# Kernel optimization log

Measured on AMD Instinct MI355X. Metric: run time of the kernel, lower is better.

The kernel has to match this reference:

```python
import jax, jax.numpy as jnp
import numpy as np

HID, NL, NH, DH, FF = 768, 12, 12, 64, 3072
VOCAB, MAXPOS = 30522, 512
T_ELE, T_ROLE = 17, 7
B, L = 16, 256
LN_EPS = 1e-12


def _layernorm(x, g, b):
    mu = x.mean(-1, keepdims=True)
    var = ((x - mu) ** 2).mean(-1, keepdims=True)
    return (x - mu) / jnp.sqrt(var + LN_EPS) * g + b


def _bert(datas, word_emb, pos_emb, type_emb, emb_ln_g, emb_ln_b,
          Wq, bq, Wk, bk, Wv, bv, Wo, bo, ln1_g, ln1_b,
          W1, b1, W2, b2, ln2_g, ln2_b):
    Bv, Lv = datas.shape
    x = word_emb[datas] + pos_emb[:Lv][None] + type_emb[0][None, None]
    x = _layernorm(x, emb_ln_g, emb_ln_b)
    for i in range(NL):  # loop over fixed layer count, not data dims
        q = (x @ Wq[i] + bq[i]).reshape(Bv, Lv, NH, DH)
        k = (x @ Wk[i] + bk[i]).reshape(Bv, Lv, NH, DH)
        v = (x @ Wv[i] + bv[i]).reshape(Bv, Lv, NH, DH)
        att = jax.nn.softmax(jnp.einsum('bqhd,bkhd->bhqk', q, k) / jnp.sqrt(jnp.float32(DH)), axis=-1)
        ctx = jnp.einsum('bhqk,bkhd->bqhd', att, v).reshape(Bv, Lv, HID)
        x = _layernorm(x + ctx @ Wo[i] + bo[i], ln1_g[i], ln1_b[i])
        h = jax.nn.gelu(x @ W1[i] + b1[i], approximate=False)
        x = _layernorm(x + h @ W2[i] + b2[i], ln2_g[i], ln2_b[i])
    return x


def _crf_llh(em, tags, mask, start, end, trans):
    # torchcrf CRF.forward with batch_first=True, reduction='sum'
    Bv, Lv, T = em.shape
    bidx = jnp.arange(Bv)
    em_t = jnp.transpose(em, (1, 0, 2))        # [L,B,T]
    tags_t = tags.T.astype(jnp.int32)          # [L,B]
    mask_t = mask.T.astype(em.dtype)           # [L,B]
    # numerator: score of gold path
    score = start[tags_t[0]] + em_t[0][bidx, tags_t[0]]
    def num_step(s, xs):
        e_t, tg, tp, m = xs
        return s + m * (trans[tp, tg] + e_t[bidx, tg]), None
    score, _ = jax.lax.scan(num_step, score, (em_t[1:], tags_t[1:], tags_t[:-1], mask_t[1:]))
    last_idx = (mask_t.sum(0) - 1).astype(jnp.int32)
    num = score + end[tags[bidx, last_idx]]
    # denominator: forward algorithm (log-sum-exp semiring)
    alpha = start[None] + em_t[0]              # [B,T]
    def den_step(a, xs):
        e_t, m = xs
        nxt = jax.nn.logsumexp(a[:, :, None] + trans[None] + e_t[:, None, :], axis=1)
        return jnp.where(m[:, None] > 0, nxt, a), None
    alpha, _ = jax.lax.scan(den_step, alpha, (em_t[1:], mask_t[1:]))
    den = jax.nn.logsumexp(alpha + end[None], axis=1)
    return jnp.sum(num - den)


def _crf_decode(em, start, end, trans):
    # torchcrf CRF.decode without mask -> full-length Viterbi
    Bv = em.shape[0]
    bidx = jnp.arange(Bv)
    em_t = jnp.transpose(em, (1, 0, 2))        # [L,B,T]
    alpha = start[None] + em_t[0]
    def fwd(a, e_t):
        sc = a[:, :, None] + trans[None]       # [B,T_prev,T_cur]
        return jnp.max(sc, axis=1) + e_t, jnp.argmax(sc, axis=1)
    alpha, hist = jax.lax.scan(fwd, alpha, em_t[1:])   # hist [L-1,B,T]
    last = jnp.argmax(alpha + end[None], axis=1)
    def back(cur, h):
        prev = h[bidx, cur]
        return prev, prev
    _, ys = jax.lax.scan(back, last, hist, reverse=True)  # ys[t] = tag at pos t
    return jnp.concatenate([ys, last[None]], axis=0).T    # [B,L]


def setup_inputs() -> dict:
    key = jax.random.key(0)
    ks = iter(jax.random.split(key, 64))
    n = lambda shape: jax.random.normal(next(ks), shape, dtype=jnp.float32) * 0.02
    inp = {
        'datas': jax.random.randint(next(ks), (B, L), 0, VOCAB, dtype=jnp.int32),
        'ele_labels': jax.random.randint(next(ks), (B, L), 0, T_ELE, dtype=jnp.int32),
        'role_labels': jax.random.randint(next(ks), (B, L), 0, T_ROLE, dtype=jnp.int32),
        'seq_mask': jnp.ones((B, L), dtype=bool),
        'word_emb': n((VOCAB, HID)), 'pos_emb': n((MAXPOS, HID)), 'type_emb': n((2, HID)),
        'emb_ln_g': jnp.ones((HID,)), 'emb_ln_b': jnp.zeros((HID,)),
        'Wq': n((NL, HID, HID)), 'bq': jnp.zeros((NL, HID)),
        'Wk': n((NL, HID, HID)), 'bk': jnp.zeros((NL, HID)),
        'Wv': n((NL, HID, HID)), 'bv': jnp.zeros((NL, HID)),
        'Wo': n((NL, HID, HID)), 'bo': jnp.zeros((NL, HID)),
        'ln1_g': jnp.ones((NL, HID)), 'ln1_b': jnp.zeros((NL, HID)),
        'W1': n((NL, HID, FF)), 'b1': jnp.zeros((NL, FF)),
        'W2': n((NL, FF, HID)), 'b2': jnp.zeros((NL, HID)),
        'ln2_g': jnp.ones((NL, HID)), 'ln2_b': jnp.zeros((NL, HID)),
        'W_ele': n((HID, T_ELE)), 'b_ele': jnp.zeros((T_ELE,)),
        'W_role': n((HID, T_ROLE)), 'b_role': jnp.zeros((T_ROLE,)),
        'ele_start': n((T_ELE,)), 'ele_end': n((T_ELE,)), 'ele_trans': n((T_ELE, T_ELE)),
        'role_start': n((T_ROLE,)), 'role_end': n((T_ROLE,)), 'role_trans': n((T_ROLE, T_ROLE)),
    }
    return inp


def reference(datas, ele_labels, role_labels, seq_mask,
              word_emb, pos_emb, type_emb, emb_ln_g, emb_ln_b,
              Wq, bq, Wk, bk, Wv, bv, Wo, bo, ln1_g, ln1_b,
              W1, b1, W2, b2, ln2_g, ln2_b,
              W_ele, b_ele, W_role, b_role,
              ele_start, ele_end, ele_trans, role_start, role_end, role_trans):
    wemb = _bert(datas, word_emb, pos_emb, type_emb, emb_ln_g, emb_ln_b,
                 Wq, bq, Wk, bk, Wv, bv, Wo, bo, ln1_g, ln1_b,
                 W1, b1, W2, b2, ln2_g, ln2_b)
    ele_em = wemb @ W_ele + b_ele
    role_em = wemb @ W_role + b_role
    mask = seq_mask.astype(jnp.float32)
    ele_llh = _crf_llh(ele_em, ele_labels, mask, ele_start, ele_end, ele_trans)
    role_llh = _crf_llh(role_em, role_labels, mask, role_start, role_end, role_trans)
    loss = -ele_llh - role_llh
    ele_dec = _crf_decode(ele_em, ele_start, ele_end, ele_trans)
    role_dec = _crf_decode(role_em, role_start, role_end, role_trans)
    return loss, ele_dec, role_dec
```

## Files before the change

### kernel.cpp

```cpp
#include <hip/hip_runtime.h>
#include <stdint.h>
#include <math.h>

typedef _Float16 f16;
typedef _Float16 f16x4 __attribute__((ext_vector_type(4)));
typedef _Float16 f16x8 __attribute__((ext_vector_type(8)));
typedef float f32x4 __attribute__((ext_vector_type(4)));

#define LO_SCALE 2048.0f
#define INV_LO_SCALE (1.0f/2048.0f)
#define LOG2E 1.4426950408889634f
#define MFMA16(a, b, c) __builtin_amdgcn_mfma_f32_16x16x32_f16(a, b, c, 0, 0, 0)

__device__ __forceinline__ void split1(float x, f16 &hi, f16 &lo) {
    f16 h = (f16)x;
    hi = h;
    lo = (f16)((x - (float)h) * LO_SCALE);
}

__device__ __forceinline__ float fexp2(float x) {
#if __has_builtin(__builtin_amdgcn_exp2f)
    return __builtin_amdgcn_exp2f(x);
#else
    return exp2f(x);
#endif
}
__device__ __forceinline__ float flog2(float x) {
#if __has_builtin(__builtin_amdgcn_logf)
    return __builtin_amdgcn_logf(x);
#else
    return log2f(x);
#endif
}

#define GLOAD16(g, l) __builtin_amdgcn_global_load_lds( \
    (const __attribute__((address_space(1))) void*)(g), \
    (__attribute__((address_space(3))) void*)(l), 16, 0, 0)

__device__ __forceinline__ void swz_decode(int &mi, int &ni)
{
    const int NN = gridDim.y;
    int s = blockIdx.x + blockIdx.y * gridDim.x;
    const int c = s & 7;
    const int idx = s >> 3;
    const int mchunk = gridDim.x >> 3;
    const int md = idx / NN;
    mi = c * mchunk + md;
    ni = idx - md * NN;
}

template<int EPI>
__device__ __forceinline__ void epi_write(float val, int row, int col, int N,
                                          float* __restrict__ C,
                                          f16* __restrict__ Oh, f16* __restrict__ Ol,
                                          f16* __restrict__ X2h, f16* __restrict__ X2l,
                                          f16* __restrict__ X3h, f16* __restrict__ X3l)
{
    if constexpr (EPI == 0) {
        C[(size_t)row * N + col] = val;
    } else if constexpr (EPI == 1) {
        float ge = 0.5f * val * (1.0f + erff(val * 0.70710678118654752440f));
        f16 hi, lo;
        split1(ge, hi, lo);
        size_t o = (size_t)row * N + col;
        Oh[o] = hi;
        Ol[o] = lo;
    } else {
        int sect = col >= 1536 ? 2 : (col >= 768 ? 1 : 0);
        int cc = col - sect * 768;
        int hd = cc >> 6;
        int d = cc & 63;
        int bh = (row >> 8) * 12 + hd;
        int lt = row & 255;
        f16 hi, lo;
        split1(val, hi, lo);
        if (sect == 0) {
            size_t o = ((size_t)bh * 256 + lt) * 64 + d;
            Oh[o] = hi; Ol[o] = lo;
        } else if (sect == 1) {
            size_t o = ((size_t)bh * 256 + lt) * 64 + d;
            X2h[o] = hi; X2l[o] = lo;
        } else {
            size_t o = ((size_t)bh * 64 + d) * 256 + lt;
            X3h[o] = hi; X3l[o] = lo;
        }
    }
}

template<int EPI>
__global__ __launch_bounds__(256, 2)
void gemm128(const f16* __restrict__ Ah, const f16* __restrict__ Al,
             const f16* __restrict__ Bh, const f16* __restrict__ Bl,
             const float* __restrict__ bias, float* __restrict__ C,
             f16* __restrict__ Oh, f16* __restrict__ Ol,
             f16* __restrict__ X2h, f16* __restrict__ X2l,
             f16* __restrict__ X3h, f16* __restrict__ X3l, int K, int N)
{
    __shared__ f16 smem[2][16384];

    int mi, ni;
    swz_decode(mi, ni);
    const int m0 = mi * 128;
    const int n0 = ni * 128;

    const int tid = threadIdx.x;
    const int lane = tid & 63;
    const int w = tid >> 6;
    const int l15 = lane & 15;
    const int lg = lane >> 4;

    f32x4 accm[4][4];
    f32x4 accc[4][4];
#pragma unroll
    for (int i = 0; i < 4; ++i)
#pragma unroll
        for (int j = 0; j < 4; ++j) {
            accm[i][j] = (f32x4){0.f, 0.f, 0.f, 0.f};
            accc[i][j] = (f32x4){0.f, 0.f, 0.f, 0.f};
        }

    const f16* gA0 = Ah + (size_t)(m0 + w * 32 + l15) * K + lg * 8;
    const f16* gA1 = gA0 + 16 * (size_t)K;
    const f16* gAl0 = Al + (size_t)(m0 + w * 32 + l15) * K + lg * 8;
    const f16* gAl1 = gAl0 + 16 * (size_t)K;
    const f16* gB0 = Bh + (size_t)(n0 + w * 32 + l15) * K + lg * 8;
    const f16* gB1 = gB0 + 16 * (size_t)K;
    const f16* gBl0 = Bl + (size_t)(n0 + w * 32 + l15) * K + lg * 8;
    const f16* gBl1 = gBl0 + 16 * (size_t)K;
    const int ldsb0 = w * 1024;
    const int ldsb1 = w * 1024 + 512;

    const int nt = K >> 5;

#define STAGE(buf, k0)                                   \
    {                                                    \
        f16* sb = &smem[buf][0];                         \
        GLOAD16(gA0 + (k0), sb + ldsb0);                 \
        GLOAD16(gA1 + (k0), sb + ldsb1);                 \
        GLOAD16(gAl0 + (k0), sb + 4096 + ldsb0);         \
        GLOAD16(gAl1 + (k0), sb + 4096 + ldsb1);         \
        GLOAD16(gB0 + (k0), sb + 8192 + ldsb0);          \
        GLOAD16(gB1 + (k0), sb + 8192 + ldsb1);          \
        GLOAD16(gBl0 + (k0), sb + 12288 + ldsb0);        \
        GLOAD16(gBl1 + (k0), sb + 12288 + ldsb1);        \
    }

    STAGE(0, 0);
    __syncthreads();

    const int fro = lg * 128 + l15 * 8;
    const int wrg = (w >> 1) * 4;
    const int wcg = (w & 1) * 4;

    int cur = 0;
    for (int t = 0; t < nt; ++t) {
        if (t + 1 < nt) STAGE(cur ^ 1, (t + 1) * 32);

        const f16* sb = &smem[cur][0];
        f16x8 fbh[4], fbl[4];
#pragma unroll
        for (int ni2 = 0; ni2 < 4; ++ni2) {
            int offb = 8192 + (wcg + ni2) * 512 + fro;
            fbh[ni2] = *(const f16x8*)(sb + offb);
            fbl[ni2] = *(const f16x8*)(sb + offb + 4096);
        }
#pragma unroll
        for (int mi2 = 0; mi2 < 4; ++mi2) {
            int offa = (wrg + mi2) * 512 + fro;
            f16x8 fah = *(const f16x8*)(sb + offa);
            f16x8 fal = *(const f16x8*)(sb + offa + 4096);
            __builtin_amdgcn_s_setprio(1);
#pragma unroll
            for (int ni2 = 0; ni2 < 4; ++ni2) {
                accm[mi2][ni2] = MFMA16(fah, fbh[ni2], accm[mi2][ni2]);
                accc[mi2][ni2] = MFMA16(fah, fbl[ni2], accc[mi2][ni2]);
                accc[mi2][ni2] = MFMA16(fal, fbh[ni2], accc[mi2][ni2]);
            }
            __builtin_amdgcn_s_setprio(0);
        }

        __syncthreads();
        cur ^= 1;
    }
#undef STAGE

    const int wr = (w >> 1) * 64;
    const int wc = (w & 1) * 64;
#pragma unroll
    for (int mi2 = 0; mi2 < 4; ++mi2) {
        int row = m0 + wr + mi2 * 16 + lg * 4;
#pragma unroll
        for (int ni2 = 0; ni2 < 4; ++ni2) {
            int col = n0 + wc + ni2 * 16 + l15;
            float bv = bias[col];
#pragma unroll
            for (int j = 0; j < 4; ++j) {
                float val = accm[mi2][ni2][j] + accc[mi2][ni2][j] * INV_LO_SCALE + bv;
                epi_write<EPI>(val, row + j, col, N, C, Oh, Ol, X2h, X2l, X3h, X3l);
            }
        }
    }
}

__global__ __launch_bounds__(256, 1)
void attn_mfma_kernel(const f16* __restrict__ Qh, const f16* __restrict__ Ql,
                      const f16* __restrict__ Kh, const f16* __restrict__ Kl,
                      const f16* __restrict__ Vth, const f16* __restrict__ Vtl,
                      f16* __restrict__ ch, f16* __restrict__ cl)
{
    __shared__ f16 sKh[256 * 72];
    __shared__ f16 sKl[256 * 72];
    __shared__ f16 sVh[64 * 264];
    __shared__ f16 sVl[64 * 264];
    __shared__ f16 sPh[4][1280];
    __shared__ f16 sPl[4][1280];

    const int bh = blockIdx.x >> 1;
    const int qbase = (blockIdx.x & 1) * 128;
    const int b = bh / 12;
    const int h = bh % 12;
    const int tid = threadIdx.x;
    const int w = tid >> 6;
    const int l = tid & 63;
    const int l15 = l & 15;
    const int lg = l >> 4;

    {
        const f16* gKh = Kh + (size_t)bh * 16384;
        const f16* gKl = Kl + (size_t)bh * 16384;
#pragma unroll
        for (int i = 0; i < 8; ++i) {
            int c = tid + i * 256;
            int off = (c >> 3) * 72 + (c & 7) * 8;
            *(f16x8*)(sKh + off) = *(const f16x8*)(gKh + c * 8);
            *(f16x8*)(sKl + off) = *(const f16x8*)(gKl + c * 8);
        }
        const f16* gVh = Vth + (size_t)bh * 16384;
        const f16* gVl = Vtl + (size_t)bh * 16384;
#pragma unroll
        for (int i = 0; i < 8; ++i) {
            int c = tid + i * 256;
            int off = (c >> 5) * 264 + (c & 31) * 8;
            *(f16x8*)(sVh + off) = *(const f16x8*)(gVh + c * 8);
            *(f16x8*)(sVl + off) = *(const f16x8*)(gVl + c * 8);
        }
    }
    __syncthreads();

    f16x8 qfh[2][2], qfl[2][2];
#pragma unroll
    for (int mt = 0; mt < 2; ++mt) {
        int qr = qbase + w * 32 + mt * 16 + l15;
        size_t qo = ((size_t)bh * 256 + qr) * 64 + lg * 8;
        qfh[mt][0] = *(const f16x8*)(Qh + qo);
        qfh[mt][1] = *(const f16x8*)(Qh + qo + 32);
        qfl[mt][0] = *(const f16x8*)(Ql + qo);
        qfl[mt][1] = *(const f16x8*)(Ql + qo + 32);
    }

    f32x4 S[2][16];
#pragma unroll
    for (int nt = 0; nt < 16; ++nt) {
        int kr = nt * 16 + l15;
        int kaddr = kr * 72 + lg * 8;
        f16x8 kh0 = *(const f16x8*)(sKh + kaddr);
        f16x8 kh1 = *(const f16x8*)(sKh + kaddr + 32);
        f16x8 kl0 = *(const f16x8*)(sKl + kaddr);
        f16x8 kl1 = *(const f16x8*)(sKl + kaddr + 32);
#pragma unroll
        for (int mt = 0; mt < 2; ++mt) {
            f32x4 am = (f32x4){0.f, 0.f, 0.f, 0.f};
            f32x4 ac = (f32x4){0.f, 0.f, 0.f, 0.f};
            am = MFMA16(qfh[mt][0], kh0, am);
            am = MFMA16(qfh[mt][1], kh1, am);
            ac = MFMA16(qfh[mt][0], kl0, ac);
            ac = MFMA16(qfh[mt][1], kl1, ac);
            ac = MFMA16(qfl[mt][0], kh0, ac);
            ac = MFMA16(qfl[mt][1], kh1, ac);
            S[mt][nt] = (am + ac * INV_LO_SCALE) * 0.125f;
        }
    }

#pragma unroll
    for (int mt = 0; mt < 2; ++mt)
#pragma unroll
        for (int j = 0; j < 4; ++j) {
            float m = S[mt][0][j];
#pragma unroll
            for (int nt = 1; nt < 16; ++nt) m = fmaxf(m, S[mt][nt][j]);
            m = fmaxf(m, __shfl_xor(m, 1));
            m = fmaxf(m, __shfl_xor(m, 2));
            m = fmaxf(m, __shfl_xor(m, 4));
            m = fmaxf(m, __shfl_xor(m, 8));
            float s = 0.f;
#pragma unroll
            for (int nt = 0; nt < 16; ++nt) {
                float e = fexp2((S[mt][nt][j] - m) * LOG2E);
                S[mt][nt][j] = e;
                s += e;
            }
            s += __shfl_xor(s, 1);
            s += __shfl_xor(s, 2);
            s += __shfl_xor(s, 4);
            s += __shfl_xor(s, 8);
            float inv = 1.0f / s;
#pragma unroll
            for (int nt = 0; nt < 16; ++nt) S[mt][nt][j] *= inv;
        }

    f32x4 Ohh[2][4], Occ[2][4];
#pragma unroll
    for (int mt = 0; mt < 2; ++mt)
#pragma unroll
        for (int dt = 0; dt < 4; ++dt) {
            Ohh[mt][dt] = (f32x4){0.f, 0.f, 0.f, 0.f};
            Occ[mt][dt] = (f32x4){0.f, 0.f, 0.f, 0.f};
        }

    f16* pbh = &sPh[w][0];
    f16* pbl = &sPl[w][0];
#pragma unroll
    for (int kp = 0; kp < 8; ++kp) {
#pragma unroll
        for (int mt = 0; mt < 2; ++mt)
#pragma unroll
            for (int n2 = 0; n2 < 2; ++n2) {
                int nt = kp * 2 + n2;
#pragma unroll
                for (int j = 0; j < 4; ++j) {
                    int prow = mt * 16 + lg * 4 + j;
                    int pcol = n2 * 16 + l15;
                    f16 hi, lo;
                    split1(S[mt][nt][j], hi, lo);
                    pbh[prow * 40 + pcol] = hi;
                    pbl[prow * 40 + pcol] = lo;
                }
            }
        __builtin_amdgcn_wave_barrier();
#pragma unroll
        for (int mt = 0; mt < 2; ++mt) {
            int paddr = (mt * 16 + l15) * 40 + lg * 8;
            f16x8 ph = *(const f16x8*)(pbh + paddr);
            f16x8 pl = *(const f16x8*)(pbl + paddr);
#pragma unroll
            for (int dt = 0; dt < 4; ++dt) {
                int vaddr = (dt * 16 + l15) * 264 + kp * 32 + lg * 8;
                f16x8 vh = *(const f16x8*)(sVh + vaddr);
                f16x8 vl = *(const f16x8*)(sVl + vaddr);
                Ohh[mt][dt] = MFMA16(ph, vh, Ohh[mt][dt]);
                Occ[mt][dt] = MFMA16(ph, vl, Occ[mt][dt]);
                Occ[mt][dt] = MFMA16(pl, vh, Occ[mt][dt]);
            }
        }
        __builtin_amdgcn_wave_barrier();
    }

#pragma unroll
    for (int mt = 0; mt < 2; ++mt)
#pragma unroll
        for (int dt = 0; dt < 4; ++dt) {
            f32x4 o = Ohh[mt][dt] + Occ[mt][dt] * INV_LO_SCALE;
#pragma unroll
            for (int j = 0; j < 4; ++j) {
                int q = qbase + w * 32 + mt * 16 + lg * 4 + j;
                int d = dt * 16 + l15;
                size_t off = ((size_t)(b * 256 + q)) * 768 + h * 64 + d;
                f16 hi, lo;
                split1(o[j], hi, lo);
                ch[off] = hi;
                cl[off] = lo;
            }
        }
}

__device__ __forceinline__ void tsplit_tile(const float* __restrict__ W,
                                            f16* __restrict__ Th, f16* __restrict__ Tl,
                                            int K, int N, int kb, int nb, int tid,
                                            float (*tile)[33])
{
    const int k0 = kb * 32;
    const int n0 = nb * 32;
    const int r = tid >> 3;
    const int c4 = (tid & 7) * 4;
    float4 v = *(const float4*)&W[(size_t)(k0 + r) * N + n0 + c4];
    tile[r][c4 + 0] = v.x; tile[r][c4 + 1] = v.y;
    tile[r][c4 + 2] = v.z; tile[r][c4 + 3] = v.w;
    __syncthreads();
    f16 hs[4], ls[4];
#pragma unroll
    for (int j = 0; j < 4; ++j) split1(tile[c4 + j][r], hs[j], ls[j]);
    size_t o = (size_t)(n0 + r) * K + k0 + c4;
    Th[o + 0] = hs[0]; Th[o + 1] = hs[1]; Th[o + 2] = hs[2]; Th[o + 3] = hs[3];
    Tl[o + 0] = ls[0]; Tl[o + 1] = ls[1]; Tl[o + 2] = ls[2]; Tl[o + 3] = ls[3];
}

#define OFF_QKV_H 0
#define OFF_QKV_L 1769472
#define OFF_WO_H  3538944
#define OFF_WO_L  4128768
#define OFF_W1_H  4718592
#define OFF_W1_L  7077888
#define OFF_W2_H  9437184
#define OFF_W2_L  11796480
#define WL_STRIDE 14155776

__global__ void tsplit_all_kernel(const float* __restrict__ Wq, const float* __restrict__ Wk,
                                  const float* __restrict__ Wv, const float* __restrict__ Wo,
                                  const float* __restrict__ W1, const float* __restrict__ W2,
                                  f16* __restrict__ wout, size_t outStride)
{
    __shared__ float tile[32][33];
    const int tid = threadIdx.x;
    const int layer = blockIdx.y;
    const size_t o768 = (size_t)layer * 589824;
    const size_t o3072 = (size_t)layer * 2359296;
    f16* base = wout + (size_t)layer * outStride;
    f16* qkvh = base + OFF_QKV_H;
    f16* qkvl = base + OFF_QKV_L;
    f16* woh  = base + OFF_WO_H;
    f16* wol  = base + OFF_WO_L;
    f16* w1h  = base + OFF_W1_H;
    f16* w1l  = base + OFF_W1_L;
    f16* w2h  = base + OFF_W2_H;
    f16* w2l  = base + OFF_W2_L;
    int bid = blockIdx.x;
    if (bid < 576) {
        tsplit_tile(Wq + o768, qkvh, qkvl, 768, 768, bid % 24, bid / 24, tid, tile);
    } else if (bid < 1152) {
        bid -= 576;
        tsplit_tile(Wk + o768, qkvh + 768 * 768, qkvl + 768 * 768, 768, 768, bid % 24, bid / 24, tid, tile);
    } else if (bid < 1728) {
        bid -= 1152;
        tsplit_tile(Wv + o768, qkvh + 2 * 768 * 768, qkvl + 2 * 768 * 768, 768, 768, bid % 24, bid / 24, tid, tile);
    } else if (bid < 2304) {
        bid -= 1728;
        tsplit_tile(Wo + o768, woh, wol, 768, 768, bid % 24, bid / 24, tid, tile);
    } else if (bid < 4608) {
        bid -= 2304;
        tsplit_tile(W1 + o3072, w1h, w1l, 768, 3072, bid % 24, bid / 24, tid, tile);
    } else {
        bid -= 4608;
        tsplit_tile(W2 + o3072, w2h, w2l, 3072, 768, bid % 96, bid / 96, tid, tile);
    }
}

__global__ void pack_qkv_bias_kernel(const float* __restrict__ bq, const float* __restrict__ bk,
                                     const float* __restrict__ bv, float* __restrict__ qkvb)
{
    const int i = blockIdx.x;
    const int tid = threadIdx.x;
    for (int c = tid; c < 768; c += 256) {
        qkvb[i * 2304 + c]        = bq[i * 768 + c];
        qkvb[i * 2304 + 768 + c]  = bk[i * 768 + c];
        qkvb[i * 2304 + 1536 + c] = bv[i * 768 + c];
    }
}

__device__ __forceinline__ void ln_wave_core(float v[12], const float* __restrict__ g,
                                             const float* __restrict__ be,
                                             float* __restrict__ x,
                                             f16* __restrict__ xh, f16* __restrict__ xl,
                                             size_t base, int cb)
{
    float s = 0.f;
#pragma unroll
    for (int j = 0; j < 12; ++j) s += v[j];
#pragma unroll
    for (int off = 32; off > 0; off >>= 1) s += __shfl_xor(s, off);
    const float mu = s * (1.0f / 768.0f);
    float d2 = 0.f;
#pragma unroll
    for (int j = 0; j < 12; ++j) { float d = v[j] - mu; d2 += d * d; }
#pragma unroll
    for (int off = 32; off > 0; off >>= 1) d2 += __shfl_xor(d2, off);
    const float rstd = 1.0f / sqrtf(d2 * (1.0f / 768.0f) + 1e-12f);

    const float4* ga = (const float4*)(g + cb);
    const float4* ba = (const float4*)(be + cb);
    float o[12];
#pragma unroll
    for (int j = 0; j < 3; ++j) {
        float4 gg = ga[j];
        float4 bb = ba[j];
        o[j * 4 + 0] = (v[j * 4 + 0] - mu) * rstd * gg.x + bb.x;
        o[j * 4 + 1] = (v[j * 4 + 1] - mu) * rstd * gg.y + bb.y;
        o[j * 4 + 2] = (v[j * 4 + 2] - mu) * rstd * gg.z + bb.z;
        o[j * 4 + 3] = (v[j * 4 + 3] - mu) * rstd * gg.w + bb.w;
    }
    float4* xo = (float4*)(x + base);
#pragma unroll
    for (int j = 0; j < 3; ++j)
        xo[j] = (float4){o[j * 4 + 0], o[j * 4 + 1], o[j * 4 + 2], o[j * 4 + 3]};

    f16 ho[12], lo[12];
#pragma unroll
    for (int j = 0; j < 12; ++j) split1(o[j], ho[j], lo[j]);
#pragma unroll
    for (int j = 0; j < 3; ++j) {
        *(f16x4*)(xh + base + j * 4) = (f16x4){ho[j * 4], ho[j * 4 + 1], ho[j * 4 + 2], ho[j * 4 + 3]};
        *(f16x4*)(xl + base + j * 4) = (f16x4){lo[j * 4], lo[j * 4 + 1], lo[j * 4 + 2], lo[j * 4 + 3]};
    }
}

__global__ __launch_bounds__(256)
void res_ln_w(float* __restrict__ x, const float* __restrict__ y,
              const float* __restrict__ g, const float* __restrict__ be,
              f16* __restrict__ xh, f16* __restrict__ xl)
{
    const int tok = blockIdx.x * 4 + (threadIdx.x >> 6);
    const int cb = (threadIdx.x & 63) * 12;
    const size_t base = (size_t)tok * 768 + cb;
    const float4* xa = (const float4*)(x + base);
    const float4* ya = (const float4*)(y + base);
    float v[12];
#pragma unroll
    for (int j = 0; j < 3; ++j) {
        float4 a = xa[j];
        float4 b2 = ya[j];
        v[j * 4 + 0] = a.x + b2.x;
        v[j * 4 + 1] = a.y + b2.y;
        v[j * 4 + 2] = a.z + b2.z;
        v[j * 4 + 3] = a.w + b2.w;
    }
    ln_wave_core(v, g, be, x, xh, xl, base, cb);
}

__global__ __launch_bounds__(256)
void embed_ln_w(const int* __restrict__ datas, const float* __restrict__ wemb,
                const float* __restrict__ pemb, const float* __restrict__ temb,
                const float* __restrict__ g, const float* __restrict__ be,
                float* __restrict__ x, f16* __restrict__ xh, f16* __restrict__ xl)
{
    const int tok = blockIdx.x * 4 + (threadIdx.x >> 6);
    const int cb = (threadIdx.x & 63) * 12;
    const size_t base = (size_t)tok * 768 + cb;
    const int widx = datas[tok];
    const int l = tok & 255;
    const float4* wa = (const float4*)(wemb + (size_t)widx * 768 + cb);
    const float4* pa = (const float4*)(pemb + (size_t)l * 768 + cb);
    const float4* ta = (const float4*)(temb + cb);
    float v[12];
#pragma unroll
    for (int j = 0; j < 3; ++j) {
        float4 a = wa[j];
        float4 b2 = pa[j];
        float4 c2 = ta[j];
        v[j * 4 + 0] = a.x + b2.x + c2.x;
        v[j * 4 + 1] = a.y + b2.y + c2.y;
        v[j * 4 + 2] = a.z + b2.z + c2.z;
        v[j * 4 + 3] = a.w + b2.w + c2.w;
    }
    ln_wave_core(v, g, be, x, xh, xl, base, cb);
}

__global__ void head_kernel(const float* __restrict__ X, const float* __restrict__ Wh,
                            const float* __restrict__ bh, float* __restrict__ out, int T)
{
    __shared__ float xs[768];
    __shared__ double part[8][32];
    const int i = blockIdx.x;
    const int tid = threadIdx.x;
    for (int c = tid; c < 768; c += 256) xs[c] = X[(size_t)i * 768 + c];
    __syncthreads();
    const int p = tid >> 5;
    const int tg = tid & 31;
    if (tg < T) {
        double a = 0;
        for (int d = p * 96; d < p * 96 + 96; ++d)
            a += (double)xs[d] * (double)Wh[d * T + tg];
        part[p][tg] = a;
    }
    __syncthreads();
    if (tid < T) {
        double s = 0;
        for (int pp = 0; pp < 8; ++pp) s += part[pp][tid];
        out[(size_t)i * T + tid] = (float)(s + (double)bh[tid]);
    }
}

__global__ void crf_num_kernel(const float* __restrict__ em, const int* __restrict__ labels,
                               const float* __restrict__ start, const float* __restrict__ endv,
                               const float* __restrict__ trans, float* __restrict__ num, int T)
{
    __shared__ double red[256];
    const int b = blockIdx.x;
    const int tid = threadIdx.x;
    const int tag = labels[b * 256 + tid];
    float v;
    if (tid == 0) {
        v = start[tag] + em[(size_t)(b * 256) * T + tag];
    } else {
        int pt = labels[b * 256 + tid - 1];
        v = trans[pt * T + tag] + em[(size_t)(b * 256 + tid) * T + tag];
    }
    red[tid] = (double)v;
    __syncthreads();
    for (int st = 128; st > 0; st >>= 1) { if (tid < st) red[tid] += red[tid + st]; __syncthreads(); }
    if (tid == 0) num[b] = (float)(red[0] + (double)endv[labels[b * 256 + 255]]);
}

template<int T>
__global__ void crf_scan_kernel(const float* __restrict__ emG, const float* __restrict__ start,
                                const float* __restrict__ endv, const float* __restrict__ trans,
                                float* __restrict__ den, float* __restrict__ tagOut)
{
    __shared__ float ems[256 * T];
    __shared__ float albuf[32];
    __shared__ unsigned char hist[255 * T + 1];
    const int b = blockIdx.x;
    const bool vit = (blockIdx.y == 1);
    const int c = threadIdx.x;

    for (int idx = c; idx < 256 * T; idx += 64)
        ems[idx] = emG[(size_t)b * 256 * T + idx];
    float trc[T];
#pragma unroll
    for (int p = 0; p < T; ++p) trc[p] = (c < T) ? trans[p * T + c] : 0.f;
    const float ec = (c < T) ? endv[c] : -1e30f;
    __syncthreads();

    float alpha = (c < T) ? (start[c] + ems[c]) : -1e30f;

    if (!vit) {
        for (int t = 1; t < 256; ++t) {
            if (c < T) albuf[c] = alpha;
            __builtin_amdgcn_wave_barrier();
            float a[T];
            float m = -1e30f;
#pragma unroll
            for (int p = 0; p < T; ++p) { a[p] = albuf[p] + trc[p]; m = fmaxf(m, a[p]); }
            float s = 0.f;
#pragma unroll
            for (int p = 0; p < T; ++p) s += fexp2((a[p] - m) * LOG2E);
            float na = m + flog2(s) * 0.6931471805599453f + ems[t * T + c];
            __builtin_amdgcn_wave_barrier();
            if (c < T) alpha = na;
        }
        if (c < T) albuf[c] = alpha + ec;
        __builtin_amdgcn_wave_barrier();
        if (c == 0) {
            float m = -1e30f;
            for (int p = 0; p < T; ++p) m = fmaxf(m, albuf[p]);
            float s = 0.f;
            for (int p = 0; p < T; ++p) s += fexp2((albuf[p] - m) * LOG2E);
            den[b] = m + flog2(s) * 0.6931471805599453f;
        }
    } else {
        for (int t = 1; t < 256; ++t) {
            if (c < T) albuf[c] = alpha;
            __builtin_amdgcn_wave_barrier();
            float best = albuf[0] + trc[0];
            int arg = 0;
#pragma unroll
            for (int p = 1; p < T; ++p) {
                float v2 = albuf[p] + trc[p];
                if (v2 > best) { best = v2; arg = p; }
            }
            __builtin_amdgcn_wave_barrier();
            if (c < T) {
                alpha = best + ems[t * T + c];
                hist[(t - 1) * T + c] = (unsigned char)arg;
            }
        }
        if (c < T) albuf[c] = alpha + ec;
        __builtin_amdgcn_wave_barrier();
        if (c == 0) {
            float bv = albuf[0];
            int cur = 0;
            for (int p = 1; p < T; ++p) {
                if (albuf[p] > bv) { bv = albuf[p]; cur = p; }
            }
            tagOut[b * 256 + 255] = (float)cur;
            for (int t = 254; t >= 0; --t) {
                cur = hist[t * T + cur];
                tagOut[b * 256 + t] = (float)cur;
            }
        }
    }
}

__global__ void loss_kernel(const float* __restrict__ num, const float* __restrict__ den,
                            float* __restrict__ out)
{
    __shared__ double red[32];
    const int tid = threadIdx.x;
    red[tid] = (double)num[tid] - (double)den[tid];
    __syncthreads();
    for (int st = 16; st > 0; st >>= 1) { if (tid < st) red[tid] += red[tid + st]; __syncthreads(); }
    if (tid == 0) out[0] = (float)(-red[0]);
}

extern "C" void kernel_launch(void* const* d_in, const int* in_sizes, int n_in,
                              void* d_out, int out_size, void* d_ws, size_t ws_size,
                              hipStream_t stream)
{
    (void)in_sizes; (void)n_in; (void)out_size;
    const int* datas       = (const int*)d_in[0];
    const int* ele_labels  = (const int*)d_in[1];
    const int* role_labels = (const int*)d_in[2];
    const float* word_emb = (const float*)d_in[4];
    const float* pos_emb  = (const float*)d_in[5];
    const float* type_emb = (const float*)d_in[6];
    const float* emb_g = (const float*)d_in[7];
    const float* emb_b = (const float*)d_in[8];
    const float* Wq = (const float*)d_in[9];  const float* bq = (const float*)d_in[10];
    const float* Wk = (const float*)d_in[11]; const float* bk = (const float*)d_in[12];
    const float* Wv = (const float*)d_in[13]; const float* bv = (const float*)d_in[14];
    const float* Wo = (const float*)d_in[15]; const float* bo = (const float*)d_in[16];
    const float* ln1g = (const float*)d_in[17]; const float* ln1b = (const float*)d_in[18];
    const float* W1 = (const float*)d_in[19]; const float* b1 = (const float*)d_in[20];
    const float* W2 = (const float*)d_in[21]; const float* b2 = (const float*)d_in[22];
    const float* ln2g = (const float*)d_in[23]; const float* ln2b = (const float*)d_in[24];
    const float* W_ele = (const float*)d_in[25]; const float* b_ele = (const float*)d_in[26];
    const float* W_role = (const float*)d_in[27]; const float* b_role = (const float*)d_in[28];
    const float* ele_start = (const float*)d_in[29];
    const float* ele_end   = (const float*)d_in[30];
    const float* ele_trans = (const float*)d_in[31];
    const float* role_start = (const float*)d_in[32];
    const float* role_end   = (const float*)d_in[33];
    const float* role_trans = (const float*)d_in[34];
    float* out = (float*)d_out;

    uint8_t* ws = (uint8_t*)d_ws;
    float* x      = (float*)(ws + 0x0000000);
    f16* xh       = (f16*)  (ws + 0x0C00000);
    f16* xl       = (f16*)  (ws + 0x1200000);
    f16* Qh       = (f16*)  (ws + 0x1800000);
    f16* Ql       = (f16*)  (ws + 0x1E00000);
    f16* Kh       = (f16*)  (ws + 0x2400000);
    f16* Kl       = (f16*)  (ws + 0x2A00000);
    f16* Vth      = (f16*)  (ws + 0x3000000);
    f16* Vtl      = (f16*)  (ws + 0x3600000);
    f16* ctxh     = (f16*)  (ws + 0x3C00000);
    f16* ctxl     = (f16*)  (ws + 0x4200000);
    float* rbuf   = (float*)(ws + 0x4800000);
    f16* hh       = (f16*)  (ws + 0x1800000);
    f16* hl       = (f16*)  (ws + 0x3000000);
    float* qkvb   = (float*)(ws + 0x5400000);
    float* ele_em = (float*)(ws + 0x5420000);
    float* role_em= (float*)(ws + 0x5468000);
    float* numb   = (float*)(ws + 0x5484000);
    float* denb   = (float*)(ws + 0x5484100);
    f16* wsplit   = (f16*)  (ws + 0x5490000);

    const bool hoist = ws_size >= (0x5490000ull + 12ull * WL_STRIDE * 2ull + 0x10000ull);

    pack_qkv_bias_kernel<<<12, 256, 0, stream>>>(bq, bk, bv, qkvb);
    embed_ln_w<<<1024, 256, 0, stream>>>(datas, word_emb, pos_emb, type_emb,
                                         emb_g, emb_b, x, xh, xl);
    if (hoist)
        tsplit_all_kernel<<<dim3(6912, 12), 256, 0, stream>>>(Wq, Wk, Wv, Wo, W1, W2,
                                                              wsplit, WL_STRIDE);

    for (int i = 0; i < 12; ++i) {
        if (!hoist)
            tsplit_all_kernel<<<dim3(6912, 1), 256, 0, stream>>>(
                Wq + (size_t)i * 589824, Wk + (size_t)i * 589824,
                Wv + (size_t)i * 589824, Wo + (size_t)i * 589824,
                W1 + (size_t)i * 2359296, W2 + (size_t)i * 2359296,
                wsplit, 0);
        f16* wl = wsplit + (hoist ? (size_t)i * WL_STRIDE : 0);

        gemm128<2><<<dim3(32, 18), 256, 0, stream>>>(xh, xl, wl + OFF_QKV_H, wl + OFF_QKV_L,
                                                     qkvb + i * 2304, nullptr,
                                                     Qh, Ql, Kh, Kl, Vth, Vtl, 768, 2304);
        attn_mfma_kernel<<<384, 256, 0, stream>>>(Qh, Ql, Kh, Kl, Vth, Vtl, ctxh, ctxl);
        gemm128<0><<<dim3(32, 6), 256, 0, stream>>>(ctxh, ctxl, wl + OFF_WO_H, wl + OFF_WO_L,
                                                    bo + i * 768, rbuf, nullptr, nullptr,
                                                    nullptr, nullptr, nullptr, nullptr, 768, 768);
        res_ln_w<<<1024, 256, 0, stream>>>(x, rbuf, ln1g + i * 768, ln1b + i * 768, xh, xl);
        gemm128<1><<<dim3(32, 24), 256, 0, stream>>>(xh, xl, wl + OFF_W1_H, wl + OFF_W1_L,
                                                     b1 + i * 3072, nullptr, hh, hl,
                                                     nullptr, nullptr, nullptr, nullptr, 768, 3072);
        gemm128<0><<<dim3(32, 6), 256, 0, stream>>>(hh, hl, wl + OFF_W2_H, wl + OFF_W2_L,
                                                    b2 + i * 768, rbuf, nullptr, nullptr,
                                                    nullptr, nullptr, nullptr, nullptr, 3072, 768);
        res_ln_w<<<1024, 256, 0, stream>>>(x, rbuf, ln2g + i * 768, ln2b + i * 768, xh, xl);
    }

    head_kernel<<<4096, 256, 0, stream>>>(x, W_ele, b_ele, ele_em, 17);
    head_kernel<<<4096, 256, 0, stream>>>(x, W_role, b_role, role_em, 7);

    crf_num_kernel<<<16, 256, 0, stream>>>(ele_em, ele_labels, ele_start, ele_end, ele_trans, numb, 17);
    crf_num_kernel<<<16, 256, 0, stream>>>(role_em, role_labels, role_start, role_end, role_trans, numb + 16, 7);
    crf_scan_kernel<17><<<dim3(16, 2), 64, 0, stream>>>(ele_em, ele_start, ele_end, ele_trans, denb, out + 1);
    crf_scan_kernel<7><<<dim3(16, 2), 64, 0, stream>>>(role_em, role_start, role_end, role_trans, denb + 16, out + 1 + 4096);
    loss_kernel<<<1, 32, 0, stream>>>(numb, denb, out);
}
```

Baseline: 5.507 ms.

## Move V transpose into attention smem load; use 64x64 weight split tiles

The QKV GEMM epilogue now writes V in the same row-major [bh, l, d] layout as Q and K, so its stores are no longer strided. The attention kernel transposes V while copying it into shared memory, using scalar LDS writes. Separately, the weight transpose-and-split kernel processes 64x64 tiles per block instead of 32x32, issuing 16-byte vector stores and launching four times fewer blocks. The trade-off is scalar, possibly bank-conflicting LDS stores in attention and a larger shared tile per block in the split kernel.

```diff
diff --git a/kernel.cpp b/kernel.cpp
--- a/kernel.cpp
+++ b/kernel.cpp
@@ -74,16 +74,10 @@
         int lt = row & 255;
         f16 hi, lo;
         split1(val, hi, lo);
-        if (sect == 0) {
-            size_t o = ((size_t)bh * 256 + lt) * 64 + d;
-            Oh[o] = hi; Ol[o] = lo;
-        } else if (sect == 1) {
-            size_t o = ((size_t)bh * 256 + lt) * 64 + d;
-            X2h[o] = hi; X2l[o] = lo;
-        } else {
-            size_t o = ((size_t)bh * 64 + d) * 256 + lt;
-            X3h[o] = hi; X3l[o] = lo;
-        }
+        size_t o = ((size_t)bh * 256 + lt) * 64 + d;
+        if (sect == 0)      { Oh[o] = hi;  Ol[o] = lo; }
+        else if (sect == 1) { X2h[o] = hi; X2l[o] = lo; }
+        else                { X3h[o] = hi; X3l[o] = lo; }
     }
 }
 
@@ -205,7 +199,7 @@
 __global__ __launch_bounds__(256, 1)
 void attn_mfma_kernel(const f16* __restrict__ Qh, const f16* __restrict__ Ql,
                       const f16* __restrict__ Kh, const f16* __restrict__ Kl,
-                      const f16* __restrict__ Vth, const f16* __restrict__ Vtl,
+                      const f16* __restrict__ Vh, const f16* __restrict__ Vl,
                       f16* __restrict__ ch, f16* __restrict__ cl)
 {
     __shared__ f16 sKh[256 * 72];
@@ -235,14 +229,20 @@
             *(f16x8*)(sKh + off) = *(const f16x8*)(gKh + c * 8);
             *(f16x8*)(sKl + off) = *(const f16x8*)(gKl + c * 8);
         }
-        const f16* gVh = Vth + (size_t)bh * 16384;
-        const f16* gVl = Vtl + (size_t)bh * 16384;
+        const f16* gVh = Vh + (size_t)bh * 16384;
+        const f16* gVl = Vl + (size_t)bh * 16384;
 #pragma unroll
         for (int i = 0; i < 8; ++i) {
             int c = tid + i * 256;
-            int off = (c >> 5) * 264 + (c & 31) * 8;
-            *(f16x8*)(sVh + off) = *(const f16x8*)(gVh + c * 8);
-            *(f16x8*)(sVl + off) = *(const f16x8*)(gVl + c * 8);
+            int l2 = c >> 3;
+            int d0 = (c & 7) * 8;
+            f16x8 vh = *(const f16x8*)(gVh + l2 * 64 + d0);
+            f16x8 vl = *(const f16x8*)(gVl + l2 * 64 + d0);
+#pragma unroll
+            for (int j = 0; j < 8; ++j) {
+                sVh[(d0 + j) * 264 + l2] = vh[j];
+                sVl[(d0 + j) * 264 + l2] = vl[j];
+            }
         }
     }
     __syncthreads();
@@ -373,25 +373,34 @@
         }
 }
 
-__device__ __forceinline__ void tsplit_tile(const float* __restrict__ W,
-                                            f16* __restrict__ Th, f16* __restrict__ Tl,
-                                            int K, int N, int kb, int nb, int tid,
-                                            float (*tile)[33])
-{
-    const int k0 = kb * 32;
-    const int n0 = nb * 32;
-    const int r = tid >> 3;
-    const int c4 = (tid & 7) * 4;
-    float4 v = *(const float4*)&W[(size_t)(k0 + r) * N + n0 + c4];
-    tile[r][c4 + 0] = v.x; tile[r][c4 + 1] = v.y;
-    tile[r][c4 + 2] = v.z; tile[r][c4 + 3] = v.w;
+__device__ __forceinline__ void tsplit64_tile(const float* __restrict__ W,
+                                              f16* __restrict__ Th, f16* __restrict__ Tl,
+                                              int K, int N, int kb, int nb, int tid,
+                                              float (*tile)[65])
+{
+    const int k0 = kb * 64;
+    const int n0 = nb * 64;
+    const int r = tid >> 2;
+    const int c16 = (tid & 3) * 16;
+#pragma unroll
+    for (int j = 0; j < 16; j += 4) {
+        float4 v = *(const float4*)&W[(size_t)(k0 + r) * N + n0 + c16 + j];
+        tile[r][c16 + j + 0] = v.x;
+        tile[r][c16 + j + 1] = v.y;
+        tile[r][c16 + j + 2] = v.z;
+        tile[r][c16 + j + 3] = v.w;
+    }
     __syncthreads();
-    f16 hs[4], ls[4];
-#pragma unroll
-    for (int j = 0; j < 4; ++j) split1(tile[c4 + j][r], hs[j], ls[j]);
-    size_t o = (size_t)(n0 + r) * K + k0 + c4;
-    Th[o + 0] = hs[0]; Th[o + 1] = hs[1]; Th[o + 2] = hs[2]; Th[o + 3] = hs[3];
-    Tl[o + 0] = ls[0]; Tl[o + 1] = ls[1]; Tl[o + 2] = ls[2]; Tl[o + 3] = ls[3];
+    const int n = tid >> 2;
+    const int k16 = (tid & 3) * 16;
+    f16 hs[16], ls[16];
+#pragma unroll
+    for (int j = 0; j < 16; ++j) split1(tile[k16 + j][n], hs[j], ls[j]);
+    size_t o = (size_t)(n0 + n) * K + k0 + k16;
+    *(f16x8*)(Th + o)     = (f16x8){hs[0], hs[1], hs[2], hs[3], hs[4], hs[5], hs[6], hs[7]};
+    *(f16x8*)(Th + o + 8) = (f16x8){hs[8], hs[9], hs[10], hs[11], hs[12], hs[13], hs[14], hs[15]};
+    *(f16x8*)(Tl + o)     = (f16x8){ls[0], ls[1], ls[2], ls[3], ls[4], ls[5], ls[6], ls[7]};
+    *(f16x8*)(Tl + o + 8) = (f16x8){ls[8], ls[9], ls[10], ls[11], ls[12], ls[13], ls[14], ls[15]};
 }
 
 #define OFF_QKV_H 0
@@ -409,38 +418,36 @@
                                   const float* __restrict__ W1, const float* __restrict__ W2,
                                   f16* __restrict__ wout, size_t outStride)
 {
-    __shared__ float tile[32][33];
+    __shared__ float tile[64][65];
     const int tid = threadIdx.x;
     const int layer = blockIdx.y;
     const size_t o768 = (size_t)layer * 589824;
     const size_t o3072 = (size_t)layer * 2359296;
     f16* base = wout + (size_t)layer * outStride;
-    f16* qkvh = base + OFF_QKV_H;
-    f16* qkvl = base + OFF_QKV_L;
-    f16* woh  = base + OFF_WO_H;
-    f16* wol  = base + OFF_WO_L;
-    f16* w1h  = base + OFF_W1_H;
-    f16* w1l  = base + OFF_W1_L;
-    f16* w2h  = base + OFF_W2_H;
-    f16* w2l  = base + OFF_W2_L;
     int bid = blockIdx.x;
-    if (bid < 576) {
-        tsplit_tile(Wq + o768, qkvh, qkvl, 768, 768, bid % 24, bid / 24, tid, tile);
+    if (bid < 144) {
+        tsplit64_tile(Wq + o768, base + OFF_QKV_H, base + OFF_QKV_L,
+                      768, 768, bid % 12, bid / 12, tid, tile);
+    } else if (bid < 288) {
+        bid -= 144;
+        tsplit64_tile(Wk + o768, base + OFF_QKV_H + 768 * 768, base + OFF_QKV_L + 768 * 768,
+                      768, 768, bid % 12, bid / 12, tid, tile);
+    } else if (bid < 432) {
+        bid -= 288;
+        tsplit64_tile(Wv + o768, base + OFF_QKV_H + 2 * 768 * 768, base + OFF_QKV_L + 2 * 768 * 768,
+                      768, 768, bid % 12, bid / 12, tid, tile);
+    } else if (bid < 576) {
+        bid -= 432;
+        tsplit64_tile(Wo + o768, base + OFF_WO_H, base + OFF_WO_L,
+                      768, 768, bid % 12, bid / 12, tid, tile);
     } else if (bid < 1152) {
         bid -= 576;
-        tsplit_tile(Wk + o768, qkvh + 768 * 768, qkvl + 768 * 768, 768, 768, bid % 24, bid / 24, tid, tile);
-    } else if (bid < 1728) {
+        tsplit64_tile(W1 + o3072, base + OFF_W1_H, base + OFF_W1_L,
+                      768, 3072, bid % 12, bid / 12, tid, tile);
+    } else {
         bid -= 1152;
-        tsplit_tile(Wv + o768, qkvh + 2 * 768 * 768, qkvl + 2 * 768 * 768, 768, 768, bid % 24, bid / 24, tid, tile);
-    } else if (bid < 2304) {
-        bid -= 1728;
-        tsplit_tile(Wo + o768, woh, wol, 768, 768, bid % 24, bid / 24, tid, tile);
-    } else if (bid < 4608) {
-        bid -= 2304;
-        tsplit_tile(W1 + o3072, w1h, w1l, 768, 3072, bid % 24, bid / 24, tid, tile);
-    } else {
-        bid -= 4608;
-        tsplit_tile(W2 + o3072, w2h, w2l, 3072, 768, bid % 96, bid / 96, tid, tile);
+        tsplit64_tile(W2 + o3072, base + OFF_W2_H, base + OFF_W2_L,
+                      3072, 768, bid % 48, bid / 48, tid, tile);
     }
 }
 
@@ -729,8 +736,8 @@
     f16* Ql       = (f16*)  (ws + 0x1E00000);
     f16* Kh       = (f16*)  (ws + 0x2400000);
     f16* Kl       = (f16*)  (ws + 0x2A00000);
-    f16* Vth      = (f16*)  (ws + 0x3000000);
-    f16* Vtl      = (f16*)  (ws + 0x3600000);
+    f16* Vh       = (f16*)  (ws + 0x3000000);
+    f16* Vl       = (f16*)  (ws + 0x3600000);
     f16* ctxh     = (f16*)  (ws + 0x3C00000);
     f16* ctxl     = (f16*)  (ws + 0x4200000);
     float* rbuf   = (float*)(ws + 0x4800000);
@@ -749,12 +756,12 @@
     embed_ln_w<<<1024, 256, 0, stream>>>(datas, word_emb, pos_emb, type_emb,
                                          emb_g, emb_b, x, xh, xl);
     if (hoist)
-        tsplit_all_kernel<<<dim3(6912, 12), 256, 0, stream>>>(Wq, Wk, Wv, Wo, W1, W2,
+        tsplit_all_kernel<<<dim3(1728, 12), 256, 0, stream>>>(Wq, Wk, Wv, Wo, W1, W2,
                                                               wsplit, WL_STRIDE);
 
     for (int i = 0; i < 12; ++i) {
         if (!hoist)
-            tsplit_all_kernel<<<dim3(6912, 1), 256, 0, stream>>>(
+            tsplit_all_kernel<<<dim3(1728, 1), 256, 0, stream>>>(
                 Wq + (size_t)i * 589824, Wk + (size_t)i * 589824,
                 Wv + (size_t)i * 589824, Wo + (size_t)i * 589824,
                 W1 + (size_t)i * 2359296, W2 + (size_t)i * 2359296,
@@ -763,8 +770,8 @@
 
         gemm128<2><<<dim3(32, 18), 256, 0, stream>>>(xh, xl, wl + OFF_QKV_H, wl + OFF_QKV_L,
                                                      qkvb + i * 2304, nullptr,
-                                                     Qh, Ql, Kh, Kl, Vth, Vtl, 768, 2304);
-        attn_mfma_kernel<<<384, 256, 0, stream>>>(Qh, Ql, Kh, Kl, Vth, Vtl, ctxh, ctxl);
+                                                     Qh, Ql, Kh, Kl, Vh, Vl, 768, 2304);
+        attn_mfma_kernel<<<384, 256, 0, stream>>>(Qh, Ql, Kh, Kl, Vh, Vl, ctxh, ctxl);
         gemm128<0><<<dim3(32, 6), 256, 0, stream>>>(ctxh, ctxl, wl + OFF_WO_H, wl + OFF_WO_L,
                                                     bo + i * 768, rbuf, nullptr, nullptr,
                                                     nullptr, nullptr, nullptr, nullptr, 768, 768);
```

Measured after the change: 5.207 ms (median of 3 runs). 5.4% less time.
